# Kernel tuning notes

Hardware: AMD Instinct MI355X
Metric: run time of the kernel (lower is better)

## Reference

```python
import jax, jax.numpy as jnp
import numpy as np

DIM = 2048
H = 16
D = DIM // H  # 128
B = 2
L = 2048


def rms_norm(x, scale):
    # torch: x.float(); rrms = rsqrt(mean(x^2)+1e-6); (x*rrms).to(dtype)*scale
    xf = x.astype(jnp.float32)
    rrms = jax.lax.rsqrt(jnp.mean(xf * xf, axis=-1, keepdims=True) + 1e-6)
    return (xf * rrms).astype(x.dtype) * scale


def apply_rope(xq, xk, pe):
    # pe: [1,1,L,D//2,2,2]; q/k: [B,H,L,D]
    xq_ = xq.astype(jnp.float32).reshape(*xq.shape[:-1], -1, 1, 2)
    xk_ = xk.astype(jnp.float32).reshape(*xk.shape[:-1], -1, 1, 2)
    xq_out = pe[..., 0] * xq_[..., 0] + pe[..., 1] * xq_[..., 1]
    xk_out = pe[..., 0] * xk_[..., 0] + pe[..., 1] * xk_[..., 1]
    return xq_out.reshape(xq.shape).astype(xq.dtype), xk_out.reshape(xk.shape).astype(xk.dtype)


def setup_inputs() -> dict:
    key = jax.random.key(0)
    ks = jax.random.split(key, 8)
    x = jax.random.normal(ks[0], (B, L, DIM), dtype=jnp.float32)
    pos_enc = jax.random.normal(ks[1], (1, 1, L, D // 2, 2, 2), dtype=jnp.float32)
    qkv_w = jax.random.normal(ks[2], (3 * DIM, DIM), dtype=jnp.float32) * (1.0 / np.sqrt(DIM))
    q_scale = jnp.ones((D,), dtype=jnp.float32)
    k_scale = jnp.ones((D,), dtype=jnp.float32)
    proj_w = jax.random.normal(ks[3], (DIM, DIM), dtype=jnp.float32) * (1.0 / np.sqrt(DIM))
    proj_b = jnp.zeros((DIM,), dtype=jnp.float32)
    return {"x": x, "pos_enc": pos_enc, "qkv_w": qkv_w, "q_scale": q_scale,
            "k_scale": k_scale, "proj_w": proj_w, "proj_b": proj_b}


def reference(x, pos_enc, qkv_w, q_scale, k_scale, proj_w, proj_b):
    b, l, dim = x.shape
    qkv = jnp.einsum('bld,ed->ble', x, qkv_w)  # [B,L,3*DIM]
    qkv = qkv.reshape(b, l, 3, H, D).transpose(2, 0, 3, 1, 4)  # [3,B,H,L,D]
    q, k, v = qkv[0], qkv[1], qkv[2]
    q = rms_norm(q, q_scale).astype(v.dtype)
    k = rms_norm(k, k_scale).astype(v.dtype)
    q, k = apply_rope(q, k, pos_enc)
    scale = 1.0 / np.sqrt(D)
    scores = jnp.einsum('bhqd,bhkd->bhqk', q, k) * scale
    probs = jax.nn.softmax(scores, axis=-1)
    o = jnp.einsum('bhqk,bhkd->bhqd', probs, v)  # [B,H,L,D]
    o = o.transpose(0, 2, 1, 3).reshape(b, l, dim)  # B H L D -> B L (H D)
    return jnp.einsum('bld,ed->ble', o, proj_w) + proj_b
```

## Files before the change

kernel.cpp:

```cpp
#include <hip/hip_runtime.h>
#include <stdint.h>

typedef unsigned short u16;
typedef short bf16x8 __attribute__((ext_vector_type(8)));
typedef float f32x4 __attribute__((ext_vector_type(4)));

#define B_   2
#define L_   2048
#define DIM_ 2048
#define H_   16
#define D_   128
#define E3_  6144
#define ML_  4096

__device__ __forceinline__ u16 f2b(float f) {
  union { float f; unsigned u; } v; v.f = f;
  return (u16)((v.u + 0x7FFFu + ((v.u >> 16) & 1u)) >> 16);
}
__device__ __forceinline__ float b2f(u16 h) {
  union { unsigned u; float f; } v; v.u = ((unsigned)h) << 16; return v.f;
}

__device__ __forceinline__ void gl_lds16(const void* g, void* l) {
  __builtin_amdgcn_global_load_lds((const __attribute__((address_space(1))) void*)g,
                                   (__attribute__((address_space(3))) void*)l, 16, 0, 0);
}

__global__ __launch_bounds__(256) void cvt_kernel(const float* __restrict__ in,
                                                  u16* __restrict__ out, int n4) {
  int i = blockIdx.x * 256 + threadIdx.x;
  int stride = gridDim.x * 256;
  for (; i < n4; i += stride) {
    float4 v = reinterpret_cast<const float4*>(in)[i];
    ushort4 o = make_ushort4(f2b(v.x), f2b(v.y), f2b(v.z), f2b(v.w));
    reinterpret_cast<ushort4*>(out)[i] = o;
  }
}

template<int OUTF32>
__global__ __launch_bounds__(256, 2) void gemm_bt(
    const u16* __restrict__ A, const u16* __restrict__ Bm,
    u16* __restrict__ Cb, float* __restrict__ Cf, const float* __restrict__ bias,
    int M, int N, int K) {
  __shared__ __align__(16) u16 As[128 * 32];
  __shared__ __align__(16) u16 Bs[128 * 32];
  const int tid = threadIdx.x;
  const int w = tid >> 6;
  const int g = (tid >> 4) & 3, r = tid & 15;
  const int wr = w >> 1, wc = w & 1;
  const long row0 = (long)blockIdx.y * 128, col0 = (long)blockIdx.x * 128;

  const f32x4 fz = {0.f, 0.f, 0.f, 0.f};
  f32x4 acc[4][4];
#pragma unroll
  for (int m = 0; m < 4; ++m)
#pragma unroll
    for (int n = 0; n < 4; ++n) acc[m][n] = fz;

  for (int k0 = 0; k0 < K; k0 += 32) {
#pragma unroll
    for (int it = 0; it < 2; ++it) {
      int c = it * 256 + tid;
      gl_lds16(A + (row0 + (c >> 2)) * (long)K + k0 + ((c & 3) << 3),
               (char*)As + ((it * 256 + (w << 6)) << 4));
      gl_lds16(Bm + (col0 + (c >> 2)) * (long)K + k0 + ((c & 3) << 3),
               (char*)Bs + ((it * 256 + (w << 6)) << 4));
    }
    __syncthreads();
    bf16x8 af[4], bfr[4];
#pragma unroll
    for (int m = 0; m < 4; ++m)
      af[m] = *reinterpret_cast<const bf16x8*>(As + (wr * 64 + m * 16 + r) * 32 + g * 8);
#pragma unroll
    for (int n = 0; n < 4; ++n)
      bfr[n] = *reinterpret_cast<const bf16x8*>(Bs + (wc * 64 + n * 16 + r) * 32 + g * 8);
#pragma unroll
    for (int m = 0; m < 4; ++m)
#pragma unroll
      for (int n = 0; n < 4; ++n)
        acc[m][n] = __builtin_amdgcn_mfma_f32_16x16x32_bf16(af[m], bfr[n], acc[m][n], 0, 0, 0);
    __syncthreads();
  }

#pragma unroll
  for (int m = 0; m < 4; ++m)
#pragma unroll
    for (int n = 0; n < 4; ++n)
#pragma unroll
      for (int j = 0; j < 4; ++j) {
        long rr = row0 + wr * 64 + m * 16 + g * 4 + j;
        long cc = col0 + wc * 64 + n * 16 + r;
        if constexpr (OUTF32) {
          Cf[rr * N + cc] = acc[m][n][j] + bias[cc];
        } else {
          Cb[rr * N + cc] = f2b(acc[m][n][j]);
        }
      }
}

__global__ __launch_bounds__(256) void normrope_kernel(
    const u16* __restrict__ qkv, const float* __restrict__ pe,
    const float* __restrict__ qsc, const float* __restrict__ ksc,
    u16* __restrict__ Qo, u16* __restrict__ Ko) {
  const int w = threadIdx.x >> 6, ln = threadIdx.x & 63;
  const int idx = blockIdx.x * 4 + w;
  const int h = idx & 15, bl = idx >> 4;
  const int l = bl & (L_ - 1), b = bl >> 11;
  const u16* base = qkv + (long)bl * E3_ + h * D_;
  const float4 pv = *reinterpret_cast<const float4*>(pe + ((long)l * 64 + ln) * 4);
  const long obase = (((long)(b * H_ + h)) * L_ + l) * D_ + 2 * ln;
  {
    unsigned qv = *reinterpret_cast<const unsigned*>(base + 2 * ln);
    float x0 = b2f((u16)qv), x1 = b2f((u16)(qv >> 16));
    float ss = x0 * x0 + x1 * x1;
#pragma unroll
    for (int msk = 1; msk < 64; msk <<= 1) ss += __shfl_xor(ss, msk);
    float rr = rsqrtf(ss * (1.0f / 128.0f) + 1e-6f);
    float y0 = x0 * rr * qsc[2 * ln], y1 = x1 * rr * qsc[2 * ln + 1];
    float o0 = pv.x * y0 + pv.y * y1, o1 = pv.z * y0 + pv.w * y1;
    *reinterpret_cast<unsigned*>(Qo + obase) = (unsigned)f2b(o0) | ((unsigned)f2b(o1) << 16);
  }
  {
    unsigned kv = *reinterpret_cast<const unsigned*>(base + DIM_ + 2 * ln);
    float x0 = b2f((u16)kv), x1 = b2f((u16)(kv >> 16));
    float ss = x0 * x0 + x1 * x1;
#pragma unroll
    for (int msk = 1; msk < 64; msk <<= 1) ss += __shfl_xor(ss, msk);
    float rr = rsqrtf(ss * (1.0f / 128.0f) + 1e-6f);
    float y0 = x0 * rr * ksc[2 * ln], y1 = x1 * rr * ksc[2 * ln + 1];
    float o0 = pv.x * y0 + pv.y * y1, o1 = pv.z * y0 + pv.w * y1;
    *reinterpret_cast<unsigned*>(Ko + obase) = (unsigned)f2b(o0) | ((unsigned)f2b(o1) << 16);
  }
}

__global__ __launch_bounds__(256) void vtrans_kernel(const u16* __restrict__ qkv,
                                                     u16* __restrict__ VT) {
  __shared__ u16 t[64][132];
  const int tid = threadIdx.x;
  const int bh = blockIdx.x >> 5, lt = blockIdx.x & 31;
  const int b = bh >> 4, h = bh & 15;
  const int l0 = lt << 6;
  const u16* src = qkv + ((long)(b * L_ + l0)) * E3_ + 2 * DIM_ + h * D_;
#pragma unroll
  for (int i = 0; i < 32; ++i) {
    int o = i * 256 + tid;
    int lr = o >> 7, d = o & 127;
    t[lr][d] = src[(long)lr * E3_ + d];
  }
  __syncthreads();
  u16* dst = VT + (long)bh * (D_ * L_) + l0;
#pragma unroll
  for (int i = 0; i < 32; ++i) {
    int o = i * 256 + tid;
    int d = o >> 6, lr = o & 63;
    dst[(long)d * L_ + lr] = t[lr][d];
  }
}

__global__ __launch_bounds__(256, 2) void flash_kernel(
    const u16* __restrict__ Qg, const u16* __restrict__ Kg,
    const u16* __restrict__ Vt, u16* __restrict__ Og) {
  __shared__ __align__(16) u16 Ks[64 * 128];
  __shared__ __align__(16) u16 Vs[128 * 64];
  __shared__ __align__(16) u16 Ps[128 * 64];
  const int tid = threadIdx.x, w = tid >> 6;
  const int g = (tid >> 4) & 3, r = tid & 15;
  const int bh = blockIdx.y, q0 = blockIdx.x * 128;
  const int b = bh >> 4, h = bh & 15;
  const u16* Qb = Qg + (long)bh * (L_ * D_);
  const u16* Kb = Kg + (long)bh * (L_ * D_);
  const u16* Vb = Vt + (long)bh * (L_ * D_);
  char* KsB = (char*)Ks; char* VsB = (char*)Vs; char* PsB = (char*)Ps;
  const float sc = 0.08838834764831845f;

  bf16x8 qf[2][4];
#pragma unroll
  for (int m = 0; m < 2; ++m)
#pragma unroll
    for (int t = 0; t < 4; ++t)
      qf[m][t] = *reinterpret_cast<const bf16x8*>(
          Qb + (long)(q0 + w * 32 + m * 16 + r) * D_ + t * 32 + g * 8);

  const f32x4 fz = {0.f, 0.f, 0.f, 0.f};
  f32x4 oacc[2][8];
  f32x4 mrun[2], lrun[2];
#pragma unroll
  for (int m = 0; m < 2; ++m) {
    mrun[m] = (f32x4){-3.0e38f, -3.0e38f, -3.0e38f, -3.0e38f};
    lrun[m] = fz;
#pragma unroll
    for (int n = 0; n < 8; ++n) oacc[m][n] = fz;
  }

  for (int kt = 0; kt < 32; ++kt) {
    const int kk0 = kt * 64;
    const u16* Ksrc = Kb + (long)kk0 * D_;
#pragma unroll
    for (int it = 0; it < 4; ++it) {
      int c = it * 256 + tid;
      int pb = c << 4;
      int krow = pb >> 8;
      int klb = (pb & 255) ^ ((krow & 7) << 4);
      gl_lds16(Ksrc + (long)krow * D_ + (klb >> 1), KsB + ((it * 256 + (w << 6)) << 4));
      int vrow = pb >> 7;
      int vlb = (pb & 127) ^ ((vrow & 7) << 4);
      gl_lds16(Vb + (long)vrow * L_ + kk0 + (vlb >> 1), VsB + ((it * 256 + (w << 6)) << 4));
    }
    __syncthreads();

    f32x4 s[2][4];
#pragma unroll
    for (int m = 0; m < 2; ++m)
#pragma unroll
      for (int n = 0; n < 4; ++n) s[m][n] = fz;
#pragma unroll
    for (int t = 0; t < 4; ++t) {
#pragma unroll
      for (int n = 0; n < 4; ++n) {
        int kr = n * 16 + r;
        bf16x8 kf = *reinterpret_cast<const bf16x8*>(
            KsB + ((kr << 8) | ((t * 64 + g * 16) ^ ((kr & 7) << 4))));
#pragma unroll
        for (int m = 0; m < 2; ++m)
          s[m][n] = __builtin_amdgcn_mfma_f32_16x16x32_bf16(qf[m][t], kf, s[m][n], 0, 0, 0);
      }
    }

#pragma unroll
    for (int m = 0; m < 2; ++m) {
      f32x4 rmx = s[m][0];
#pragma unroll
      for (int n = 1; n < 4; ++n)
#pragma unroll
        for (int j = 0; j < 4; ++j) rmx[j] = fmaxf(rmx[j], s[m][n][j]);
#pragma unroll
      for (int j = 0; j < 4; ++j) {
#pragma unroll
        for (int msk = 1; msk < 16; msk <<= 1)
          rmx[j] = fmaxf(rmx[j], __shfl_xor(rmx[j], msk));
      }
      f32x4 mnew, corr, rsum;
#pragma unroll
      for (int j = 0; j < 4; ++j) {
        mnew[j] = fmaxf(mrun[m][j], rmx[j] * sc);
        corr[j] = __expf(mrun[m][j] - mnew[j]);
        rsum[j] = 0.f;
      }
#pragma unroll
      for (int n = 0; n < 4; ++n) {
#pragma unroll
        for (int j = 0; j < 4; ++j) {
          float p = __expf(s[m][n][j] * sc - mnew[j]);
          rsum[j] += p;
          int ql = w * 32 + m * 16 + g * 4 + j;
          int col = n * 16 + r;
          *reinterpret_cast<u16*>(PsB + ((ql << 7) | ((col << 1) ^ ((ql & 7) << 4)))) = f2b(p);
        }
      }
#pragma unroll
      for (int j = 0; j < 4; ++j) {
#pragma unroll
        for (int msk = 1; msk < 16; msk <<= 1) rsum[j] += __shfl_xor(rsum[j], msk);
        lrun[m][j] = lrun[m][j] * corr[j] + rsum[j];
      }
      mrun[m] = mnew;
#pragma unroll
      for (int n = 0; n < 8; ++n)
#pragma unroll
        for (int j = 0; j < 4; ++j) oacc[m][n][j] *= corr[j];
    }

#pragma unroll
    for (int t = 0; t < 2; ++t) {
      bf16x8 pf[2];
#pragma unroll
      for (int m = 0; m < 2; ++m) {
        int pr = w * 32 + m * 16 + r;
        pf[m] = *reinterpret_cast<const bf16x8*>(
            PsB + ((pr << 7) | ((t * 64 + g * 16) ^ ((pr & 7) << 4))));
      }
#pragma unroll
      for (int n = 0; n < 8; ++n) {
        int vr = n * 16 + r;
        bf16x8 vf = *reinterpret_cast<const bf16x8*>(
            VsB + ((vr << 7) | ((t * 64 + g * 16) ^ ((vr & 7) << 4))));
#pragma unroll
        for (int m = 0; m < 2; ++m)
          oacc[m][n] = __builtin_amdgcn_mfma_f32_16x16x32_bf16(pf[m], vf, oacc[m][n], 0, 0, 0);
      }
    }
    __syncthreads();
  }

#pragma unroll
  for (int m = 0; m < 2; ++m) {
    f32x4 inv;
#pragma unroll
    for (int j = 0; j < 4; ++j) inv[j] = 1.0f / lrun[m][j];
#pragma unroll
    for (int n = 0; n < 8; ++n)
#pragma unroll
      for (int j = 0; j < 4; ++j) {
        int ql = w * 32 + m * 16 + g * 4 + j;
        int col = n * 16 + r;
        Og[((long)(b * L_) + q0 + ql) * DIM_ + h * D_ + col] = f2b(oacc[m][n][j] * inv[j]);
      }
  }
}

extern "C" void kernel_launch(void* const* d_in, const int* in_sizes, int n_in,
                              void* d_out, int out_size, void* d_ws, size_t ws_size,
                              hipStream_t stream) {
  const float* x    = (const float*)d_in[0];
  const float* pe   = (const float*)d_in[1];
  const float* qkvw = (const float*)d_in[2];
  const float* qsc  = (const float*)d_in[3];
  const float* ksc  = (const float*)d_in[4];
  const float* pw   = (const float*)d_in[5];
  const float* pb   = (const float*)d_in[6];
  float* out = (float*)d_out;

  u16* ws_x   = (u16*)d_ws;
  u16* ws_w1  = ws_x   + (size_t)ML_ * DIM_;
  u16* ws_w2  = ws_w1  + (size_t)E3_ * DIM_;
  u16* ws_qkv = ws_w2  + (size_t)DIM_ * DIM_;
  u16* ws_q   = ws_qkv + (size_t)ML_ * E3_;
  u16* ws_k   = ws_q   + (size_t)ML_ * DIM_;
  u16* ws_vt  = ws_k   + (size_t)ML_ * DIM_;
  u16* ws_o   = ws_vt  + (size_t)ML_ * DIM_;

  cvt_kernel<<<2048, 256, 0, stream>>>(x, ws_x, ML_ * DIM_ / 4);
  cvt_kernel<<<2048, 256, 0, stream>>>(qkvw, ws_w1, E3_ * DIM_ / 4);
  cvt_kernel<<<2048, 256, 0, stream>>>(pw, ws_w2, DIM_ * DIM_ / 4);

  gemm_bt<0><<<dim3(E3_ / 128, ML_ / 128), 256, 0, stream>>>(
      ws_x, ws_w1, ws_qkv, nullptr, nullptr, ML_, E3_, DIM_);
  normrope_kernel<<<(B_ * L_ * H_) / 4, 256, 0, stream>>>(ws_qkv, pe, qsc, ksc, ws_q, ws_k);
  vtrans_kernel<<<B_ * H_ * (L_ / 64), 256, 0, stream>>>(ws_qkv, ws_vt);
  flash_kernel<<<dim3(L_ / 128, B_ * H_), 256, 0, stream>>>(ws_q, ws_k, ws_vt, ws_o);
  gemm_bt<1><<<dim3(DIM_ / 128, ML_ / 128), 256, 0, stream>>>(
      ws_o, ws_w2, nullptr, out, pb, ML_, DIM_, DIM_);
}
```

Baseline: 491.6 us.

## Double-buffer K/V tiles, add lazy softmax rescaling, and raise MFMA priority

The flash attention loop now keeps two LDS buffers for K and V. The next tile's global-to-LDS loads are issued before the current tile is computed, and the per-iteration syncthreads is replaced by a vmcnt wait plus a barrier at the end of the loop, so loads overlap compute. The online softmax now rescales the running max, sum and output accumulators only when some row's max grows by more than 8; otherwise it keeps the stale max, which avoids the exp and rescale multiplies on most tiles. MFMA sections are wrapped in s_setprio to favour matrix issue. LDS use rises from 48KB to 80KB per block, which may limit occupancy, and the lazy rescale lets unnormalised probabilities reach up to about e^8.

```diff
diff --git a/kernel.cpp b/kernel.cpp
--- a/kernel.cpp
+++ b/kernel.cpp
@@ -160,8 +160,8 @@
 __global__ __launch_bounds__(256, 2) void flash_kernel(
     const u16* __restrict__ Qg, const u16* __restrict__ Kg,
     const u16* __restrict__ Vt, u16* __restrict__ Og) {
-  __shared__ __align__(16) u16 Ks[64 * 128];
-  __shared__ __align__(16) u16 Vs[128 * 64];
+  __shared__ __align__(16) u16 Ks[2][64 * 128];
+  __shared__ __align__(16) u16 Vs[2][128 * 64];
   __shared__ __align__(16) u16 Ps[128 * 64];
   const int tid = threadIdx.x, w = tid >> 6;
   const int g = (tid >> 4) & 3, r = tid & 15;
@@ -170,7 +170,7 @@
   const u16* Qb = Qg + (long)bh * (L_ * D_);
   const u16* Kb = Kg + (long)bh * (L_ * D_);
   const u16* Vb = Vt + (long)bh * (L_ * D_);
-  char* KsB = (char*)Ks; char* VsB = (char*)Vs; char* PsB = (char*)Ps;
+  char* PsB = (char*)Ps;
   const float sc = 0.08838834764831845f;
 
   bf16x8 qf[2][4];
@@ -192,9 +192,11 @@
     for (int n = 0; n < 8; ++n) oacc[m][n] = fz;
   }
 
-  for (int kt = 0; kt < 32; ++kt) {
+  auto stage = [&](int buf, int kt) {
     const int kk0 = kt * 64;
     const u16* Ksrc = Kb + (long)kk0 * D_;
+    char* KsB = (char*)Ks[buf];
+    char* VsB = (char*)Vs[buf];
 #pragma unroll
     for (int it = 0; it < 4; ++it) {
       int c = it * 256 + tid;
@@ -206,13 +208,24 @@
       int vlb = (pb & 127) ^ ((vrow & 7) << 4);
       gl_lds16(Vb + (long)vrow * L_ + kk0 + (vlb >> 1), VsB + ((it * 256 + (w << 6)) << 4));
     }
-    __syncthreads();
+  };
+
+  stage(0, 0);
+  asm volatile("s_waitcnt vmcnt(0)" ::: "memory");
+  __builtin_amdgcn_s_barrier();
+
+  for (int kt = 0; kt < 32; ++kt) {
+    const int cur = kt & 1;
+    if (kt + 1 < 32) stage(cur ^ 1, kt + 1);
+    const char* KsB = (const char*)Ks[cur];
+    const char* VsB = (const char*)Vs[cur];
 
     f32x4 s[2][4];
 #pragma unroll
     for (int m = 0; m < 2; ++m)
 #pragma unroll
       for (int n = 0; n < 4; ++n) s[m][n] = fz;
+    __builtin_amdgcn_s_setprio(1);
 #pragma unroll
     for (int t = 0; t < 4; ++t) {
 #pragma unroll
@@ -225,6 +238,7 @@
           s[m][n] = __builtin_amdgcn_mfma_f32_16x16x32_bf16(qf[m][t], kf, s[m][n], 0, 0, 0);
       }
     }
+    __builtin_amdgcn_s_setprio(0);
 
 #pragma unroll
     for (int m = 0; m < 2; ++m) {
@@ -239,18 +253,26 @@
         for (int msk = 1; msk < 16; msk <<= 1)
           rmx[j] = fmaxf(rmx[j], __shfl_xor(rmx[j], msk));
       }
-      f32x4 mnew, corr, rsum;
-#pragma unroll
-      for (int j = 0; j < 4; ++j) {
-        mnew[j] = fmaxf(mrun[m][j], rmx[j] * sc);
-        corr[j] = __expf(mrun[m][j] - mnew[j]);
-        rsum[j] = 0.f;
-      }
+      float growth = rmx[0] * sc - mrun[m][0];
+#pragma unroll
+      for (int j = 1; j < 4; ++j) growth = fmaxf(growth, rmx[j] * sc - mrun[m][j]);
+      if (!__all(growth <= 8.0f)) {
+#pragma unroll
+        for (int j = 0; j < 4; ++j) {
+          float mnew = fmaxf(mrun[m][j], rmx[j] * sc);
+          float corr = __expf(mrun[m][j] - mnew);
+          mrun[m][j] = mnew;
+          lrun[m][j] *= corr;
+#pragma unroll
+          for (int n = 0; n < 8; ++n) oacc[m][n][j] *= corr;
+        }
+      }
+      f32x4 rsum = fz;
 #pragma unroll
       for (int n = 0; n < 4; ++n) {
 #pragma unroll
         for (int j = 0; j < 4; ++j) {
-          float p = __expf(s[m][n][j] * sc - mnew[j]);
+          float p = __expf(s[m][n][j] * sc - mrun[m][j]);
           rsum[j] += p;
           int ql = w * 32 + m * 16 + g * 4 + j;
           int col = n * 16 + r;
@@ -261,15 +283,11 @@
       for (int j = 0; j < 4; ++j) {
 #pragma unroll
         for (int msk = 1; msk < 16; msk <<= 1) rsum[j] += __shfl_xor(rsum[j], msk);
-        lrun[m][j] = lrun[m][j] * corr[j] + rsum[j];
-      }
-      mrun[m] = mnew;
-#pragma unroll
-      for (int n = 0; n < 8; ++n)
-#pragma unroll
-        for (int j = 0; j < 4; ++j) oacc[m][n][j] *= corr[j];
-    }
-
+        lrun[m][j] += rsum[j];
+      }
+    }
+
+    __builtin_amdgcn_s_setprio(1);
 #pragma unroll
     for (int t = 0; t < 2; ++t) {
       bf16x8 pf[2];
@@ -289,7 +307,10 @@
           oacc[m][n] = __builtin_amdgcn_mfma_f32_16x16x32_bf16(pf[m], vf, oacc[m][n], 0, 0, 0);
       }
     }
-    __syncthreads();
+    __builtin_amdgcn_s_setprio(0);
+
+    asm volatile("s_waitcnt vmcnt(0)" ::: "memory");
+    __builtin_amdgcn_s_barrier();
   }
 
 #pragma unroll
```

Result: no change. 483.1 us (-1.7%).
